# Kernel tuning notes

Measured on AMD Instinct MI355X. Metric: run time of the kernel, lower is better.

## Reference

```python
import jax, jax.numpy as jnp
import numpy as np
from jax import lax

H = 1024  # hidden_size
L = 2     # num_layers


def gru_cell(x, h, Wih, Whh, bih, bhh):
    # PyTorch GRU gate order: r, z, n
    gi = x @ Wih.T + bih          # [B, 3H]
    gh = h @ Whh.T + bhh          # [B, 3H]
    ir, iz, inn = jnp.split(gi, 3, axis=-1)
    hr, hz, hn = jnp.split(gh, 3, axis=-1)
    r = jax.nn.sigmoid(ir + hr)
    z = jax.nn.sigmoid(iz + hz)
    n = jnp.tanh(inn + r * hn)
    return (1.0 - z) * n + z * h


def stacked_step(h, x_t, layers):
    # h: [L, B, H]; x_t: [B, in]; layers: list of (Wih, Whh, bih, bhh)
    hs = []
    inp = x_t
    for l, (Wih, Whh, bih, bhh) in enumerate(layers):
        hl = gru_cell(inp, h[l], Wih, Whh, bih, bhh)
        hs.append(hl)
        inp = hl
    return jnp.stack(hs), inp  # new hidden stack, top-layer output


def run_gru_seq(x_seq, h0, layers):
    # x_seq: [B, S, in] -> scan over time
    def step(h, x_t):
        h_new, out = stacked_step(h, x_t, layers)
        return h_new, out
    h_final, outs = lax.scan(step, h0, jnp.transpose(x_seq, (1, 0, 2)))
    return outs[-1], h_final  # last-timestep top-layer output [B, H]


def setup_inputs() -> dict:
    key = jax.random.key(0)
    ks = jax.random.split(key, 10)
    B, S = 128, 256

    def xavier(k, shape):
        fan_out, fan_in = shape
        std = np.sqrt(2.0 / (fan_in + fan_out))
        return jax.random.normal(k, shape, dtype=jnp.float32) * std

    inp = {
        "x": jax.random.normal(ks[0], (B, S), dtype=jnp.float32),
        "h0": jax.random.uniform(ks[1], (L, B, H), dtype=jnp.float32) * 0.01,
        "Wih0": xavier(ks[2], (3 * H, 1)),
        "Whh0": xavier(ks[3], (3 * H, H)),
        "bih0": jnp.zeros((3 * H,), jnp.float32),
        "bhh0": jnp.zeros((3 * H,), jnp.float32),
        "Wih1": xavier(ks[4], (3 * H, H)),
        "Whh1": xavier(ks[5], (3 * H, H)),
        "bih1": jnp.zeros((3 * H,), jnp.float32),
        "bhh1": jnp.zeros((3 * H,), jnp.float32),
        "fc_w": jax.random.uniform(ks[6], (1, H), jnp.float32, -1.0 / np.sqrt(H), 1.0 / np.sqrt(H)),
        "fc_b": jax.random.uniform(ks[7], (1,), jnp.float32, -1.0 / np.sqrt(H), 1.0 / np.sqrt(H)),
        "forcast_length": 8,
    }
    return inp


def reference(x, h0, Wih0, Whh0, bih0, bhh0, Wih1, Whh1, bih1, bhh1, fc_w, fc_b, forcast_length):
    layers = [(Wih0, Whh0, bih0, bhh0), (Wih1, Whh1, bih1, bhh1)]

    # forecast step i=0: full conditioning sequence
    out0, h = run_gru_seq(x[..., None], h0, layers)   # [B, H], [L, B, H]
    y0 = out0 @ fc_w.T + fc_b                          # [B, 1]

    def fstep(carry, _):
        xc, hc = carry                                 # xc: [B, 1]
        h_new, out = stacked_step(hc, xc, layers)
        y = out @ fc_w.T + fc_b                        # [B, 1]
        return (y, h_new), y[:, 0]

    (y_last, h_final), ys = lax.scan(fstep, (y0, h), None, length=forcast_length - 1)
    forcast_out = jnp.concatenate([y0[:, 0][None, :], ys], axis=0)  # [F, B]
    return jnp.mean(forcast_out, axis=0), h_final
```

## Files before the change

kernel.cpp:

```cpp
#include <hip/hip_runtime.h>

#define NB 128
#define NH 1024
#define NS 256
#define NF 8
#define NBLK 192
#define NTH 512
#define AG  __HIP_MEMORY_SCOPE_AGENT

#define GLOBL 0
#define RELL  64
#define INITL 128
#define XCNT  192
#define XARR  512
#define XCPY  1024

typedef _Float16 half_t;
typedef _Float16 f16x8 __attribute__((ext_vector_type(8)));
typedef float f32x4 __attribute__((ext_vector_type(4)));
typedef unsigned long long u64;

struct GP {
    const float *x, *hin, *Wih0, *Whh0, *bih0, *bhh0, *Wih1, *Whh1, *bih1, *bhh1, *fcw, *fcb;
    float *ypart, *out;
    half_t *h0b0, *h0b1, *h1b0, *h1b1;
    char *reg;
    unsigned *bar;
};

__device__ __forceinline__ float fast_sigmoid(float x) { return 1.0f / (1.0f + __expf(-x)); }
__device__ __forceinline__ float fast_tanh(float x) {
    float e = __expf(2.0f * x);
    return (e - 1.0f) / (e + 1.0f);
}

__device__ __forceinline__ u64 ldu64(const void* p) {
    return __hip_atomic_load((const u64*)p, __ATOMIC_RELAXED, AG);
}
__device__ __forceinline__ void stu64(void* p, u64 v) {
    __hip_atomic_store((u64*)p, v, __ATOMIC_RELAXED, AG);
}
__device__ __forceinline__ float ldf32(const float* p) {
    return __hip_atomic_load(p, __ATOMIC_RELAXED, AG);
}
__device__ __forceinline__ void stf32(float* p, float v) {
    __hip_atomic_store(p, v, __ATOMIC_RELAXED, AG);
}
__device__ __forceinline__ unsigned aadd(unsigned* p, unsigned v) {
    return __hip_atomic_fetch_add(p, v, __ATOMIC_RELAXED, AG);
}
__device__ __forceinline__ unsigned ald(const unsigned* p) {
    return __hip_atomic_load(p, __ATOMIC_RELAXED, AG);
}

__device__ __forceinline__ void l2add(unsigned* p, unsigned v) {
    asm volatile("global_atomic_add %0, %1, off" :: "v"(p), "v"(v) : "memory");
}
__device__ __forceinline__ unsigned l2add_rtn(unsigned* p, unsigned v) {
    unsigned ret;
    asm volatile("global_atomic_add %0, %1, %2, off sc0\n\ts_waitcnt vmcnt(0)"
                 : "=v"(ret) : "v"(p), "v"(v) : "memory");
    return ret;
}

__global__ void k_init(const float* __restrict__ hin, half_t* __restrict__ h0h,
                       half_t* __restrict__ h1h) {
    int i = blockIdx.x * 256 + threadIdx.x;
    h0h[i] = (half_t)hin[i];
    h1h[i] = (half_t)hin[NB * NH + i];
}

__global__ __launch_bounds__(NTH)
void k_gru(GP p) {
    extern __shared__ char lds[];
    const int tid = threadIdx.x;
    const int l   = tid & 63;
    const int wv  = tid >> 6;
    const int bid = blockIdx.x;
    const int role = (bid < 64) ? 0 : 1;
    const int lc   = bid - 64;
    const int colbase = role ? lc * 8 : bid * 16;
    float* hl  = (float*)(lds + 98304);
    int* meta  = (int*)(lds + 106496);
    unsigned* bar = p.bar;

    const int cloc = l & 15;
    const int col8 = cloc & 7;

    {
        for (int i = tid; i < 12288; i += NTH) {
            int row = i >> 8, j = i & 255;
            const float* Wsrc;
            int wrow;
            if (role == 0) {
                Wsrc = p.Whh0; wrow = (row >> 4) * NH + colbase + (row & 15);
            } else {
                int plane = row >> 3, cl = row & 7;
                Wsrc = (plane < 3) ? p.Wih1 : p.Whh1;
                int g = (plane < 3) ? plane : plane - 3;
                wrow = g * NH + colbase + cl;
            }
            float4 v = *(const float4*)(Wsrc + (size_t)wrow * NH + j * 4);
            union { half_t h[4]; uint2 u; } cv;
            cv.h[0] = (half_t)v.x; cv.h[1] = (half_t)v.y;
            cv.h[2] = (half_t)v.z; cv.h[3] = (half_t)v.w;
            *(uint2*)(lds + (row * 2048 + ((j * 8) ^ ((row & 7) << 4)))) = cv.u;
        }
        if (role == 0) {
            for (int i = tid; i < NB * 16; i += NTH)
                hl[i] = p.hin[(size_t)(i >> 4) * NH + colbase + (i & 15)];
        } else {
            for (int i = tid; i < NB * 8; i += NTH)
                hl[i] = p.hin[(size_t)NB * NH + (size_t)(i >> 3) * NH + colbase + (i & 7)];
        }
    }

    if (tid == 0) {
        unsigned x;
        asm volatile("s_getreg_b32 %0, hwreg(HW_REG_XCC_ID)" : "=s"(x));
        x &= 7;
        unsigned r = aadd(bar + XCNT + x * 32, 1u);
        asm volatile("s_waitcnt vmcnt(0)" ::: "memory");
        aadd(bar + INITL, 1u);
        while (ald(bar + INITL) < NBLK) __builtin_amdgcn_s_sleep(1);
        int nn = 0, cnt = 0;
        for (int k = 0; k < 8; ++k) {
            unsigned c = ald(bar + XCNT + k * 32);
            if (c) ++cnt;
            if (k == (int)x) nn = (int)c;
        }
        meta[0] = (int)x; meta[1] = (int)r; meta[2] = nn; meta[3] = cnt;
    }
    __syncthreads();
    const int xcd_  = meta[0];
    const int rank_ = meta[1];
    const int n_    = meta[2];
    const int nx_   = meta[3];

    float bi_[3] = {0,0,0}, bh_[3] = {0,0,0}, wx_[3] = {0,0,0}, fcwv = 0.f, fcb_ = 0.f;
    float bi_lo = 0.f, bh_lo = 0.f, bi2 = 0.f, bh2 = 0.f;
    if (role == 0) {
        int c = colbase + cloc;
        #pragma unroll
        for (int g = 0; g < 3; ++g) {
            bi_[g] = p.bih0[g * NH + c]; bh_[g] = p.bhh0[g * NH + c];
            wx_[g] = p.Wih0[g * NH + c];
        }
        fcb_ = p.fcb[0];
    } else {
        int glo = cloc >> 3;
        int c8 = colbase + col8;
        bi_lo = p.bih1[glo * NH + c8]; bh_lo = p.bhh1[glo * NH + c8];
        bi2   = p.bih1[2 * NH + c8];   bh2   = p.bhh1[2 * NH + c8];
        fcwv  = p.fcw[c8];
    }

    const int rb_l0[3] = { cloc * 2048, (16 + cloc) * 2048, (32 + cloc) * 2048 };
    const int rb_l1[4] = { cloc * 2048, (16 + col8) * 2048, (24 + cloc) * 2048, (40 + col8) * 2048 };
    const int rmask = (col8) << 4;
    const int kb0 = (l >> 4) << 4;
    const int arow = wv * 16 + cloc;
    const int b0base = wv * 16 + ((l >> 4) << 2);
    const int aloff = (l >> 4) * 2048 + arow * 16;

    auto gbar = [&](unsigned t) {
        __syncthreads();
        if (tid == 0) {
            l2add(bar + XARR + xcd_ * 32, 1u);
            if (rank_ == 0) {
                while (l2add_rtn(bar + XARR + xcd_ * 32, 0u) < (unsigned)n_ * t)
                    __builtin_amdgcn_s_sleep(1);
                unsigned old = aadd(bar + GLOBL, 1u);
                if (old == (unsigned)nx_ * t - 1u) aadd(bar + RELL, 1u);
            }
            while (ald(bar + RELL) < t) __builtin_amdgcn_s_sleep(1);
        }
        __syncthreads();
        asm volatile("buffer_inv" ::: "memory");
    };

    auto xcopy = [&](const half_t* h0s, const half_t* h1s, int slot) {
        char* dst = p.reg + ((size_t)(xcd_ * 2 + slot)) * 524288;
        for (int idx = rank_ * NTH + tid; idx < 32768; idx += n_ * NTH) {
            int which = idx >> 14, kq = (idx >> 7) & 127, row = idx & 127;
            const half_t* s = (which ? h1s : h0s) + row * 1024 + kq * 8;
            union { u64 u[2]; uint4 v; } t;
            t.u[0] = ldu64(s);
            t.u[1] = ldu64(s + 4);
            *(uint4*)(dst + which * 262144 + (size_t)(kq * 128 + row) * 16) = t.v;
        }
    };
    auto csync = [&](unsigned ct) {
        __syncthreads();
        if (tid == 0) {
            l2add(bar + XCPY + xcd_ * 32, 1u);
            while (l2add_rtn(bar + XCPY + xcd_ * 32, 0u) < (unsigned)n_ * ct)
                __builtin_amdgcn_s_sleep(1);
        }
        __syncthreads();
    };

    auto gemm_l0 = [&](const char* regA, f32x4 (&acc)[3]) {
        const char* ap = regA + aloff;
        #pragma unroll 8
        for (int ks = 0; ks < 32; ++ks) {
            f16x8 a = *(const f16x8*)(ap + (size_t)ks * 8192);
            int kb = ks * 64 + kb0;
            #pragma unroll
            for (int g = 0; g < 3; ++g) {
                f16x8 bf = *(const f16x8*)(lds + rb_l0[g] + (kb ^ rmask));
                acc[g] = __builtin_amdgcn_mfma_f32_16x16x32_f16(a, bf, acc[g], 0, 0, 0);
            }
        }
    };

    auto gemm_l1 = [&](const char* regA, f32x4 (&acc)[4]) {
        const char* ap0 = regA + aloff;
        const char* ap1 = regA + 262144 + aloff;
        #pragma unroll 8
        for (int ks = 0; ks < 32; ++ks) {
            f16x8 a0 = *(const f16x8*)(ap0 + (size_t)ks * 8192);
            f16x8 a1 = *(const f16x8*)(ap1 + (size_t)ks * 8192);
            int kb = ks * 64 + kb0;
            f16x8 b0 = *(const f16x8*)(lds + rb_l1[0] + (kb ^ rmask));
            acc[0] = __builtin_amdgcn_mfma_f32_16x16x32_f16(a0, b0, acc[0], 0, 0, 0);
            f16x8 b1 = *(const f16x8*)(lds + rb_l1[1] + (kb ^ rmask));
            acc[1] = __builtin_amdgcn_mfma_f32_16x16x32_f16(a0, b1, acc[1], 0, 0, 0);
            f16x8 b2 = *(const f16x8*)(lds + rb_l1[2] + (kb ^ rmask));
            acc[2] = __builtin_amdgcn_mfma_f32_16x16x32_f16(a1, b2, acc[2], 0, 0, 0);
            f16x8 b3 = *(const f16x8*)(lds + rb_l1[3] + (kb ^ rmask));
            acc[3] = __builtin_amdgcn_mfma_f32_16x16x32_f16(a1, b3, acc[3], 0, 0, 0);
        }
    };

    auto pack_store16 = [&](half_t* hw, int b, float hn) {
        unsigned v = (unsigned)__builtin_bit_cast(unsigned short, (half_t)hn);
        unsigned o = __shfl_xor(v, 1);
        unsigned pair = (l & 1) ? (o | (v << 16)) : (v | (o << 16));
        unsigned p2 = __shfl_xor(pair, 2);
        u64 quad = (l & 2) ? (((u64)pair << 32) | p2) : ((u64)pair | ((u64)p2 << 32));
        if ((l & 3) == 0) stu64(hw + (size_t)b * NH + ((colbase + cloc) & ~3), quad);
    };

    auto l0_epi = [&](const float xv[4], f32x4 (&acc)[3], half_t* hw) {
        #pragma unroll
        for (int q = 0; q < 4; ++q) {
            int b = b0base + q;
            float gh0 = acc[0][q] + bh_[0];
            float gh1 = acc[1][q] + bh_[1];
            float gh2 = acc[2][q] + bh_[2];
            float r_ = fast_sigmoid(xv[q] * wx_[0] + bi_[0] + gh0);
            float z_ = fast_sigmoid(xv[q] * wx_[1] + bi_[1] + gh1);
            float n_2 = fast_tanh(xv[q] * wx_[2] + bi_[2] + r_ * gh2);
            float hp = hl[b * 16 + cloc];
            float hn = (1.0f - z_) * n_2 + z_ * hp;
            hl[b * 16 + cloc] = hn;
            pack_store16(hw, b, hn);
        }
    };

    auto l1_epi = [&](f32x4 (&acc)[4], half_t* hw, float* ydst) {
        #pragma unroll
        for (int q = 0; q < 4; ++q) {
            int b = b0base + q;
            float rz = fast_sigmoid(acc[0][q] + bi_lo + acc[2][q] + bh_lo);
            float zv = __shfl_xor(rz, 8);
            float n_2 = fast_tanh(acc[1][q] + bi2 + rz * (acc[3][q] + bh2));
            float hp = hl[b * 8 + col8];
            float hn = (1.0f - zv) * n_2 + zv * hp;
            if (cloc < 8) hl[b * 8 + col8] = hn;
            unsigned v = (unsigned)__builtin_bit_cast(unsigned short, (half_t)hn);
            unsigned o = __shfl_xor(v, 1);
            unsigned pair = (l & 1) ? (o | (v << 16)) : (v | (o << 16));
            unsigned p2 = __shfl_xor(pair, 2);
            u64 quad = (l & 2) ? (((u64)pair << 32) | p2) : ((u64)pair | ((u64)p2 << 32));
            if ((l & 3) == 0 && cloc < 8)
                stu64(hw + (size_t)b * NH + ((colbase + col8) & ~3), quad);
            if (ydst) {
                float s = hn * fcwv;
                s += __shfl_xor(s, 1);
                s += __shfl_xor(s, 2);
                s += __shfl_xor(s, 4);
                if (cloc == 0) stf32(ydst + lc * NB + b, s);
            }
        }
    };

    auto reduce_y = [&](float xv[4]) {
        #pragma unroll
        for (int q = 0; q < 4; ++q) {
            int b = b0base + q;
            float t0 = ldf32(p.ypart + (cloc * 8 + 0) * NB + b);
            float t1 = ldf32(p.ypart + (cloc * 8 + 1) * NB + b);
            float t2 = ldf32(p.ypart + (cloc * 8 + 2) * NB + b);
            float t3 = ldf32(p.ypart + (cloc * 8 + 3) * NB + b);
            float t4 = ldf32(p.ypart + (cloc * 8 + 4) * NB + b);
            float t5 = ldf32(p.ypart + (cloc * 8 + 5) * NB + b);
            float t6 = ldf32(p.ypart + (cloc * 8 + 6) * NB + b);
            float t7 = ldf32(p.ypart + (cloc * 8 + 7) * NB + b);
            xv[q] = ((t0 + t1) + (t2 + t3)) + ((t4 + t5) + (t6 + t7));
        }
        #pragma unroll
        for (int m = 1; m < 16; m <<= 1) {
            xv[0] += __shfl_xor(xv[0], m); xv[1] += __shfl_xor(xv[1], m);
            xv[2] += __shfl_xor(xv[2], m); xv[3] += __shfl_xor(xv[3], m);
        }
        #pragma unroll
        for (int q = 0; q < 4; ++q) xv[q] += fcb_;
    };

    unsigned tgt = 0, ctgt = 0;
    int cur0 = 0, cur1 = 0;
    f32x4 zero4 = {0.f, 0.f, 0.f, 0.f};
    float ysum[4] = {0.f, 0.f, 0.f, 0.f};

    auto COPY = [&]() {
        ++ctgt;
        int slot = (int)(ctgt & 1);
        xcopy(cur0 ? p.h0b1 : p.h0b0, cur1 ? p.h1b1 : p.h1b0, slot);
        csync(ctgt);
        return (const char*)(p.reg + (size_t)(xcd_ * 2 + slot) * 524288);
    };

    for (int ph = 0; ph <= NS; ++ph) {
        float xv[4];
        if (role == 0 && ph < NS) {
            #pragma unroll
            for (int q = 0; q < 4; ++q) xv[q] = p.x[(size_t)(b0base + q) * NS + ph];
        }
        const char* regB = COPY();
        if (role == 0 && ph < NS) {
            f32x4 acc[3] = {zero4, zero4, zero4};
            gemm_l0(regB, acc);
            l0_epi(xv, acc, cur0 ? p.h0b0 : p.h0b1);
        } else if (role == 1 && ph >= 1) {
            f32x4 acc[4] = {zero4, zero4, zero4, zero4};
            gemm_l1(regB, acc);
            l1_epi(acc, cur1 ? p.h1b0 : p.h1b1, (ph == NS) ? p.ypart : nullptr);
        }
        ++tgt; gbar(tgt);
        if (ph < NS) cur0 ^= 1;
        if (ph >= 1) cur1 ^= 1;
    }

    for (int i = 1; i < NF; ++i) {
        float xv[4];
        if (role == 0) {
            reduce_y(xv);
            #pragma unroll
            for (int q = 0; q < 4; ++q) ysum[q] += xv[q];
        }
        const char* regB = COPY();
        if (role == 0) {
            f32x4 acc[3] = {zero4, zero4, zero4};
            gemm_l0(regB, acc);
            l0_epi(xv, acc, cur0 ? p.h0b0 : p.h0b1);
        }
        ++tgt; gbar(tgt); cur0 ^= 1;

        regB = COPY();
        if (role == 1) {
            f32x4 acc[4] = {zero4, zero4, zero4, zero4};
            gemm_l1(regB, acc);
            l1_epi(acc, cur1 ? p.h1b0 : p.h1b1, p.ypart);
        }
        ++tgt; gbar(tgt); cur1 ^= 1;
    }

    if (role == 0) {
        float y7[4];
        reduce_y(y7);
        if (bid == 0 && cloc == 0) {
            #pragma unroll
            for (int q = 0; q < 4; ++q)
                p.out[b0base + q] = (ysum[q] + y7[q]) * 0.125f;
        }
        float* ob = p.out + NB;
        for (int i = tid; i < NB * 16; i += NTH)
            ob[(size_t)(i >> 4) * NH + colbase + (i & 15)] = hl[i];
    } else {
        float* ob = p.out + NB + (size_t)NB * NH;
        for (int i = tid; i < NB * 8; i += NTH)
            ob[(size_t)(i >> 3) * NH + colbase + (i & 7)] = hl[i];
    }
}

extern "C" void kernel_launch(void* const* d_in, const int* in_sizes, int n_in,
                              void* d_out, int out_size, void* d_ws, size_t ws_size,
                              hipStream_t stream)
{
    GP p;
    p.x    = (const float*)d_in[0];
    p.hin  = (const float*)d_in[1];
    p.Wih0 = (const float*)d_in[2];
    p.Whh0 = (const float*)d_in[3];
    p.bih0 = (const float*)d_in[4];
    p.bhh0 = (const float*)d_in[5];
    p.Wih1 = (const float*)d_in[6];
    p.Whh1 = (const float*)d_in[7];
    p.bih1 = (const float*)d_in[8];
    p.bhh1 = (const float*)d_in[9];
    p.fcw  = (const float*)d_in[10];
    p.fcb  = (const float*)d_in[11];
    p.out  = (float*)d_out;

    char* ws = (char*)d_ws;
    p.bar   = (unsigned*)ws;                     ws += 8192;
    p.h0b0  = (half_t*)ws;                       ws += 262144;
    p.h0b1  = (half_t*)ws;                       ws += 262144;
    p.h1b0  = (half_t*)ws;                       ws += 262144;
    p.h1b1  = (half_t*)ws;                       ws += 262144;
    p.ypart = (float*)ws;                        ws += 65536;
    ws = (char*)(((size_t)ws + 4095) & ~(size_t)4095);
    p.reg   = ws;                                ws += 8 * 2 * 524288;

    hipMemsetAsync(p.bar, 0, 8192, stream);
    k_init<<<512, 256, 0, stream>>>(p.hin, p.h0b0, p.h1b0);

    void* args[] = { &p };
    if (hipLaunchCooperativeKernel((void*)k_gru, dim3(NBLK), dim3(NTH), args,
                                   106752, stream) != hipSuccess) {
        (void)hipGetLastError();
        k_gru<<<dim3(NBLK), dim3(NTH), 106752, stream>>>(p);
    }
}
```

Baseline: 3.844 ms.

## Split-K GEMM across wave pairs, flatten grid barrier, batch xcopy loads

Waves are regrouped into 4 M-tiles of 32 rows times 2 K-halves. Each wave now computes two 16-row MFMA tiles over half of K, so every B fragment read from LDS is reused twice, and the two K-halves are combined through an LDS reduction buffer. The hierarchical per-XCD grid barrier is replaced with a flat global atomic counter, and xcopy issues its first three loads before any stores to increase memory-level parallelism. The changes cost a larger shared-memory footprint, an extra __syncthreads per step, and more contention on a single global atomic.

```diff
diff --git a/kernel.cpp b/kernel.cpp
--- a/kernel.cpp
+++ b/kernel.cpp
@@ -12,7 +12,6 @@
 #define RELL  64
 #define INITL 128
 #define XCNT  192
-#define XARR  512
 #define XCPY  1024
 
 typedef _Float16 half_t;
@@ -76,12 +75,15 @@
     const int tid = threadIdx.x;
     const int l   = tid & 63;
     const int wv  = tid >> 6;
+    const int mh  = wv & 3;
+    const int kh  = wv >> 2;
     const int bid = blockIdx.x;
     const int role = (bid < 64) ? 0 : 1;
     const int lc   = bid - 64;
     const int colbase = role ? lc * 8 : bid * 16;
     float* hl  = (float*)(lds + 98304);
     int* meta  = (int*)(lds + 106496);
+    float* red = (float*)(lds + 106752);
     unsigned* bar = p.bar;
 
     const int cloc = l & 15;
@@ -123,19 +125,15 @@
         asm volatile("s_waitcnt vmcnt(0)" ::: "memory");
         aadd(bar + INITL, 1u);
         while (ald(bar + INITL) < NBLK) __builtin_amdgcn_s_sleep(1);
-        int nn = 0, cnt = 0;
-        for (int k = 0; k < 8; ++k) {
-            unsigned c = ald(bar + XCNT + k * 32);
-            if (c) ++cnt;
-            if (k == (int)x) nn = (int)c;
-        }
-        meta[0] = (int)x; meta[1] = (int)r; meta[2] = nn; meta[3] = cnt;
+        int nn = 0;
+        unsigned cv_ = ald(bar + XCNT + x * 32);
+        nn = (int)cv_;
+        meta[0] = (int)x; meta[1] = (int)r; meta[2] = nn;
     }
     __syncthreads();
     const int xcd_  = meta[0];
     const int rank_ = meta[1];
     const int n_    = meta[2];
-    const int nx_   = meta[3];
 
     float bi_[3] = {0,0,0}, bh_[3] = {0,0,0}, wx_[3] = {0,0,0}, fcwv = 0.f, fcb_ = 0.f;
     float bi_lo = 0.f, bh_lo = 0.f, bi2 = 0.f, bh2 = 0.f;
@@ -157,22 +155,16 @@
 
     const int rb_l0[3] = { cloc * 2048, (16 + cloc) * 2048, (32 + cloc) * 2048 };
     const int rb_l1[4] = { cloc * 2048, (16 + col8) * 2048, (24 + cloc) * 2048, (40 + col8) * 2048 };
-    const int rmask = (col8) << 4;
-    const int kb0 = (l >> 4) << 4;
-    const int arow = wv * 16 + cloc;
-    const int b0base = wv * 16 + ((l >> 4) << 2);
-    const int aloff = (l >> 4) * 2048 + arow * 16;
+    const int rmask = col8 << 4;
+    const int kb_base = kh * 1024 + ((l >> 4) << 4);
+    const int bsel = mh * 32 + kh * 16 + ((l >> 4) << 2);
+    const int aloff = (kh * 64 + (l >> 4)) * 2048 + (mh * 32 + cloc) * 16;
 
     auto gbar = [&](unsigned t) {
         __syncthreads();
         if (tid == 0) {
-            l2add(bar + XARR + xcd_ * 32, 1u);
-            if (rank_ == 0) {
-                while (l2add_rtn(bar + XARR + xcd_ * 32, 0u) < (unsigned)n_ * t)
-                    __builtin_amdgcn_s_sleep(1);
-                unsigned old = aadd(bar + GLOBL, 1u);
-                if (old == (unsigned)nx_ * t - 1u) aadd(bar + RELL, 1u);
-            }
+            unsigned old = aadd(bar + GLOBL, 1u);
+            if (old == (unsigned)NBLK * t - 1u) aadd(bar + RELL, 1u);
             while (ald(bar + RELL) < t) __builtin_amdgcn_s_sleep(1);
         }
         __syncthreads();
@@ -181,13 +173,30 @@
 
     auto xcopy = [&](const half_t* h0s, const half_t* h1s, int slot) {
         char* dst = p.reg + ((size_t)(xcd_ * 2 + slot)) * 524288;
-        for (int idx = rank_ * NTH + tid; idx < 32768; idx += n_ * NTH) {
+        const int stride = n_ * NTH;
+        int i0 = rank_ * NTH + tid, i1 = i0 + stride, i2 = i1 + stride;
+        auto srcp = [&](int idx) {
             int which = idx >> 14, kq = (idx >> 7) & 127, row = idx & 127;
-            const half_t* s = (which ? h1s : h0s) + row * 1024 + kq * 8;
-            union { u64 u[2]; uint4 v; } t;
-            t.u[0] = ldu64(s);
-            t.u[1] = ldu64(s + 4);
-            *(uint4*)(dst + which * 262144 + (size_t)(kq * 128 + row) * 16) = t.v;
+            return (const half_t*)((which ? h1s : h0s) + row * 1024 + kq * 8);
+        };
+        auto dstp = [&](int idx) {
+            int which = idx >> 14, kq = (idx >> 7) & 127, row = idx & 127;
+            return dst + which * 262144 + (size_t)(kq * 128 + row) * 16;
+        };
+        bool v0 = i0 < 32768, v1 = i1 < 32768, v2 = i2 < 32768;
+        u64 a0, b0, a1, b1, a2, b2;
+        const half_t *s0 = srcp(v0 ? i0 : 0), *s1 = srcp(v1 ? i1 : 0), *s2 = srcp(v2 ? i2 : 0);
+        if (v0) { a0 = ldu64(s0); b0 = ldu64(s0 + 4); }
+        if (v1) { a1 = ldu64(s1); b1 = ldu64(s1 + 4); }
+        if (v2) { a2 = ldu64(s2); b2 = ldu64(s2 + 4); }
+        if (v0) { char* d = dstp(i0); *(u64*)d = a0; *(u64*)(d + 8) = b0; }
+        if (v1) { char* d = dstp(i1); *(u64*)d = a1; *(u64*)(d + 8) = b1; }
+        if (v2) { char* d = dstp(i2); *(u64*)d = a2; *(u64*)(d + 8) = b2; }
+        for (int idx = i0 + 3 * stride; idx < 32768; idx += stride) {
+            const half_t* s = srcp(idx);
+            u64 xa = ldu64(s), xb = ldu64(s + 4);
+            char* d = dstp(idx);
+            *(u64*)d = xa; *(u64*)(d + 8) = xb;
         }
     };
     auto csync = [&](unsigned ct) {
@@ -200,38 +209,49 @@
         __syncthreads();
     };
 
-    auto gemm_l0 = [&](const char* regA, f32x4 (&acc)[3]) {
+    auto gemm_l0 = [&](const char* regA, f32x4 (&acc)[2][3]) {
         const char* ap = regA + aloff;
         #pragma unroll 8
-        for (int ks = 0; ks < 32; ++ks) {
-            f16x8 a = *(const f16x8*)(ap + (size_t)ks * 8192);
-            int kb = ks * 64 + kb0;
+        for (int ks = 0; ks < 16; ++ks) {
+            f16x8 a0 = *(const f16x8*)(ap + ks * 8192);
+            f16x8 a1 = *(const f16x8*)(ap + ks * 8192 + 256);
+            int kb = kb_base + ks * 64;
             #pragma unroll
             for (int g = 0; g < 3; ++g) {
                 f16x8 bf = *(const f16x8*)(lds + rb_l0[g] + (kb ^ rmask));
-                acc[g] = __builtin_amdgcn_mfma_f32_16x16x32_f16(a, bf, acc[g], 0, 0, 0);
+                acc[0][g] = __builtin_amdgcn_mfma_f32_16x16x32_f16(a0, bf, acc[0][g], 0, 0, 0);
+                acc[1][g] = __builtin_amdgcn_mfma_f32_16x16x32_f16(a1, bf, acc[1][g], 0, 0, 0);
             }
         }
     };
 
-    auto gemm_l1 = [&](const char* regA, f32x4 (&acc)[4]) {
+    auto gemm_l1 = [&](const char* regA, f32x4 (&acc)[2][4]) {
         const char* ap0 = regA + aloff;
         const char* ap1 = regA + 262144 + aloff;
-        #pragma unroll 8
-        for (int ks = 0; ks < 32; ++ks) {
-            f16x8 a0 = *(const f16x8*)(ap0 + (size_t)ks * 8192);
-            f16x8 a1 = *(const f16x8*)(ap1 + (size_t)ks * 8192);
-            int kb = ks * 64 + kb0;
+        #pragma unroll 4
+        for (int ks = 0; ks < 16; ++ks) {
+            f16x8 a00 = *(const f16x8*)(ap0 + ks * 8192);
+            f16x8 a01 = *(const f16x8*)(ap0 + ks * 8192 + 256);
+            f16x8 a10 = *(const f16x8*)(ap1 + ks * 8192);
+            f16x8 a11 = *(const f16x8*)(ap1 + ks * 8192 + 256);
+            int kb = kb_base + ks * 64;
             f16x8 b0 = *(const f16x8*)(lds + rb_l1[0] + (kb ^ rmask));
-            acc[0] = __builtin_amdgcn_mfma_f32_16x16x32_f16(a0, b0, acc[0], 0, 0, 0);
+            acc[0][0] = __builtin_amdgcn_mfma_f32_16x16x32_f16(a00, b0, acc[0][0], 0, 0, 0);
+            acc[1][0] = __builtin_amdgcn_mfma_f32_16x16x32_f16(a01, b0, acc[1][0], 0, 0, 0);
             f16x8 b1 = *(const f16x8*)(lds + rb_l1[1] + (kb ^ rmask));
-            acc[1] = __builtin_amdgcn_mfma_f32_16x16x32_f16(a0, b1, acc[1], 0, 0, 0);
+            acc[0][1] = __builtin_amdgcn_mfma_f32_16x16x32_f16(a00, b1, acc[0][1], 0, 0, 0);
+            acc[1][1] = __builtin_amdgcn_mfma_f32_16x16x32_f16(a01, b1, acc[1][1], 0, 0, 0);
             f16x8 b2 = *(const f16x8*)(lds + rb_l1[2] + (kb ^ rmask));
-            acc[2] = __builtin_amdgcn_mfma_f32_16x16x32_f16(a1, b2, acc[2], 0, 0, 0);
+            acc[0][2] = __builtin_amdgcn_mfma_f32_16x16x32_f16(a10, b2, acc[0][2], 0, 0, 0);
+            acc[1][2] = __builtin_amdgcn_mfma_f32_16x16x32_f16(a11, b2, acc[1][2], 0, 0, 0);
             f16x8 b3 = *(const f16x8*)(lds + rb_l1[3] + (kb ^ rmask));
-            acc[3] = __builtin_amdgcn_mfma_f32_16x16x32_f16(a1, b3, acc[3], 0, 0, 0);
-        }
-    };
+            acc[0][3] = __builtin_amdgcn_mfma_f32_16x16x32_f16(a10, b3, acc[0][3], 0, 0, 0);
+            acc[1][3] = __builtin_amdgcn_mfma_f32_16x16x32_f16(a11, b3, acc[1][3], 0, 0, 0);
+        }
+    };
+
+    float* redw = red + mh * 2048 + kh * 1024 + (l << 2);
+    float* redr = red + mh * 2048 + (kh ^ 1) * 1024 + (l << 2);
 
     auto pack_store16 = [&](half_t* hw, int b, float hn) {
         unsigned v = (unsigned)__builtin_bit_cast(unsigned short, (half_t)hn);
@@ -245,7 +265,7 @@
     auto l0_epi = [&](const float xv[4], f32x4 (&acc)[3], half_t* hw) {
         #pragma unroll
         for (int q = 0; q < 4; ++q) {
-            int b = b0base + q;
+            int b = bsel + q;
             float gh0 = acc[0][q] + bh_[0];
             float gh1 = acc[1][q] + bh_[1];
             float gh2 = acc[2][q] + bh_[2];
@@ -262,7 +282,7 @@
     auto l1_epi = [&](f32x4 (&acc)[4], half_t* hw, float* ydst) {
         #pragma unroll
         for (int q = 0; q < 4; ++q) {
-            int b = b0base + q;
+            int b = bsel + q;
             float rz = fast_sigmoid(acc[0][q] + bi_lo + acc[2][q] + bh_lo);
             float zv = __shfl_xor(rz, 8);
             float n_2 = fast_tanh(acc[1][q] + bi2 + rz * (acc[3][q] + bh2));
@@ -289,24 +309,16 @@
     auto reduce_y = [&](float xv[4]) {
         #pragma unroll
         for (int q = 0; q < 4; ++q) {
-            int b = b0base + q;
-            float t0 = ldf32(p.ypart + (cloc * 8 + 0) * NB + b);
-            float t1 = ldf32(p.ypart + (cloc * 8 + 1) * NB + b);
-            float t2 = ldf32(p.ypart + (cloc * 8 + 2) * NB + b);
-            float t3 = ldf32(p.ypart + (cloc * 8 + 3) * NB + b);
-            float t4 = ldf32(p.ypart + (cloc * 8 + 4) * NB + b);
-            float t5 = ldf32(p.ypart + (cloc * 8 + 5) * NB + b);
-            float t6 = ldf32(p.ypart + (cloc * 8 + 6) * NB + b);
-            float t7 = ldf32(p.ypart + (cloc * 8 + 7) * NB + b);
-            xv[q] = ((t0 + t1) + (t2 + t3)) + ((t4 + t5) + (t6 + t7));
-        }
-        #pragma unroll
-        for (int m = 1; m < 16; m <<= 1) {
-            xv[0] += __shfl_xor(xv[0], m); xv[1] += __shfl_xor(xv[1], m);
-            xv[2] += __shfl_xor(xv[2], m); xv[3] += __shfl_xor(xv[3], m);
-        }
-        #pragma unroll
-        for (int q = 0; q < 4; ++q) xv[q] += fcb_;
+            int b = bsel + q;
+            float t[8];
+            #pragma unroll
+            for (int j = 0; j < 8; ++j)
+                t[j] = ldf32(p.ypart + (cloc * 8 + j) * NB + b);
+            float s = ((t[0] + t[1]) + (t[2] + t[3])) + ((t[4] + t[5]) + (t[6] + t[7]));
+            #pragma unroll
+            for (int mm = 1; mm < 16; mm <<= 1) s += __shfl_xor(s, mm);
+            xv[q] = s + fcb_;
+        }
     };
 
     unsigned tgt = 0, ctgt = 0;
@@ -322,21 +334,51 @@
         return (const char*)(p.reg + (size_t)(xcd_ * 2 + slot) * 524288);
     };
 
+    auto do_l0 = [&](const float xv[4], const char* regB, half_t* hw) {
+        f32x4 acc[2][3];
+        #pragma unroll
+        for (int m = 0; m < 2; ++m) { acc[m][0] = zero4; acc[m][1] = zero4; acc[m][2] = zero4; }
+        gemm_l0(regB, acc);
+        #pragma unroll
+        for (int g = 0; g < 3; ++g)
+            *(f32x4*)(redw + g * 256) = acc[kh ^ 1][g];
+        __syncthreads();
+        f32x4 own[3];
+        #pragma unroll
+        for (int g = 0; g < 3; ++g)
+            own[g] = acc[kh][g] + *(const f32x4*)(redr + g * 256);
+        l0_epi(xv, own, hw);
+    };
+    auto do_l1 = [&](const char* regB, half_t* hw, float* ydst) {
+        f32x4 acc[2][4];
+        #pragma unroll
+        for (int m = 0; m < 2; ++m)
+            #pragma unroll
+            for (int g = 0; g < 4; ++g) acc[m][g] = zero4;
+        gemm_l1(regB, acc);
+        #pragma unroll
+        for (int g = 0; g < 4; ++g)
+            *(f32x4*)(redw + g * 256) = acc[kh ^ 1][g];
+        __syncthreads();
+        f32x4 own[4];
+        #pragma unroll
+        for (int g = 0; g < 4; ++g)
+            own[g] = acc[kh][g] + *(const f32x4*)(redr + g * 256);
+        l1_epi(own, hw, ydst);
+    };
+
     for (int ph = 0; ph <= NS; ++ph) {
         float xv[4];
         if (role == 0 && ph < NS) {
             #pragma unroll
-            for (int q = 0; q < 4; ++q) xv[q] = p.x[(size_t)(b0base + q) * NS + ph];
+            for (int q = 0; q < 4; ++q)
+                xv[q] = p.x[(size_t)(bsel + q) * NS + ph];
         }
         const char* regB = COPY();
         if (role == 0 && ph < NS) {
-            f32x4 acc[3] = {zero4, zero4, zero4};
-            gemm_l0(regB, acc);
-            l0_epi(xv, acc, cur0 ? p.h0b0 : p.h0b1);
+            do_l0(xv, regB, cur0 ? p.h0b0 : p.h0b1);
         } else if (role == 1 && ph >= 1) {
-            f32x4 acc[4] = {zero4, zero4, zero4, zero4};
-            gemm_l1(regB, acc);
-            l1_epi(acc, cur1 ? p.h1b0 : p.h1b1, (ph == NS) ? p.ypart : nullptr);
+            do_l1(regB, cur1 ? p.h1b0 : p.h1b1, (ph == NS) ? p.ypart : nullptr);
         }
         ++tgt; gbar(tgt);
         if (ph < NS) cur0 ^= 1;
@@ -351,19 +393,11 @@
             for (int q = 0; q < 4; ++q) ysum[q] += xv[q];
         }
         const char* regB = COPY();
-        if (role == 0) {
-            f32x4 acc[3] = {zero4, zero4, zero4};
-            gemm_l0(regB, acc);
-            l0_epi(xv, acc, cur0 ? p.h0b0 : p.h0b1);
-        }
+        if (role == 0) do_l0(xv, regB, cur0 ? p.h0b0 : p.h0b1);
         ++tgt; gbar(tgt); cur0 ^= 1;
 
         regB = COPY();
-        if (role == 1) {
-            f32x4 acc[4] = {zero4, zero4, zero4, zero4};
-            gemm_l1(regB, acc);
-            l1_epi(acc, cur1 ? p.h1b0 : p.h1b1, p.ypart);
-        }
+        if (role == 1) do_l1(regB, cur1 ? p.h1b0 : p.h1b1, p.ypart);
         ++tgt; gbar(tgt); cur1 ^= 1;
     }
 
@@ -373,7 +407,7 @@
         if (bid == 0 && cloc == 0) {
             #pragma unroll
             for (int q = 0; q < 4; ++q)
-                p.out[b0base + q] = (ysum[q] + y7[q]) * 0.125f;
+                p.out[bsel + q] = (ysum[q] + y7[q]) * 0.125f;
         }
         float* ob = p.out + NB;
         for (int i = tid; i < NB * 16; i += NTH)
@@ -419,8 +453,8 @@
 
     void* args[] = { &p };
     if (hipLaunchCooperativeKernel((void*)k_gru, dim3(NBLK), dim3(NTH), args,
-                                   106752, stream) != hipSuccess) {
+                                   139520, stream) != hipSuccess) {
         (void)hipGetLastError();
-        k_gru<<<dim3(NBLK), dim3(NTH), 106752, stream>>>(p);
-    }
-}
+        k_gru<<<dim3(NBLK), dim3(NTH), 139520, stream>>>(p);
+    }
+}
```

After: 6.197 ms. 61.2% more time.
